# Optimization experiments

Measured on AMD Instinct MI355X. Metric: run time of the kernel, lower is better.

The kernel has to match this reference:

```python
import jax, jax.numpy as jnp
import numpy as np

D_MODEL = 1024
M = 4
NUM_EXPERTS = 8
TOP_K = 2
B, T = 2, 2048


def setup_inputs() -> dict:
    key = jax.random.key(0)
    ks = jax.random.split(key, 4)
    d_ff = D_MODEL * M
    x = jax.random.normal(ks[0], (B, T, D_MODEL), dtype=jnp.float32)
    # torch nn.Linear(d_model, num_experts, bias=False): stored here as (D, E) so logits = x @ gate_w
    gate_w = jax.random.normal(ks[1], (D_MODEL, NUM_EXPERTS), dtype=jnp.float32) * 0.02
    w1 = jax.random.normal(ks[2], (NUM_EXPERTS, D_MODEL, d_ff), dtype=jnp.float32) * 0.02
    b1 = jnp.zeros((NUM_EXPERTS, d_ff), dtype=jnp.float32)
    w2 = jax.random.normal(ks[3], (NUM_EXPERTS, d_ff, D_MODEL), dtype=jnp.float32) * 0.02
    b2 = jnp.zeros((NUM_EXPERTS, D_MODEL), dtype=jnp.float32)
    return {"x": x, "gate_w": gate_w, "w1": w1, "b1": b1, "w2": w2, "b2": b2}


def reference(x, gate_w, w1, b1, w2, b2):
    Bb, Tt, D = x.shape
    E = w1.shape[0]
    N = Bb * Tt
    # gating: top-k logits -> softmax over the k selected experts
    logits = jnp.einsum('btd,de->bte', x, gate_w)               # (B,T,E)
    top_v, top_i = jax.lax.top_k(logits, TOP_K)                 # (B,T,K)
    top_w = jax.nn.softmax(top_v, axis=-1)                      # (B,T,K)

    xf = x.reshape(N, D)
    idx = top_i.reshape(N, TOP_K)
    wts = top_w.reshape(N, TOP_K)
    # dense combine weights: comb[n, e] = sum_k wts[n,k] * [idx[n,k]==e]
    comb = jnp.zeros((N, E), dtype=x.dtype).at[jnp.arange(N)[:, None], idx].add(wts)

    # per-expert dense 2-layer MLP (exact erf GELU, matching torch F.gelu default),
    # combined with gate weights (zero weight == token not routed to expert).
    out = jnp.zeros((N, D), dtype=x.dtype)
    for e in range(E):
        h = jax.nn.gelu(xf @ w1[e] + b1[e], approximate=False)  # (N, D*M)
        out = out + comb[:, e:e + 1] * (h @ w2[e] + b2[e])      # (N, D)
    return out.reshape(Bb, Tt, D)
```

## Files before the change

### kernel.cpp

```cpp
#include <hip/hip_runtime.h>
#include <hip/hip_bf16.h>
#include <math.h>

#define D_MODEL 1024
#define D_FF    4096
#define NEXP    8
#define NTOK    4096
#define NROUTED 8192

typedef __attribute__((ext_vector_type(8))) short bf16x8;
typedef __attribute__((ext_vector_type(4))) float f32x4;
typedef __attribute__((ext_vector_type(4))) unsigned short us4;

#define WS_CNT   0
#define WS_CNT2  64
#define WS_OFF   128
#define WS_TI    256
#define WS_TW    (WS_TI + NTOK*2*4)
#define WS_TOK   (WS_TW + NTOK*2*4)
#define WS_GWT   (WS_TOK + NROUTED*4)
#define WS_XG    (((WS_GWT + NROUTED*4) + 255) & ~255)
#define WS_H     (WS_XG + (size_t)NROUTED*D_MODEL*2)
#define WS_WT    (WS_H + (size_t)NROUTED*D_FF*2)

__device__ __forceinline__ unsigned short f2bf(float f){
  union { float f; unsigned u; } a; a.f = f;
  unsigned u = a.u;
  u = u + 0x7FFF + ((u >> 16) & 1);
  return (unsigned short)(u >> 16);
}

__device__ __forceinline__ void gload_lds16(const void* g, void* l){
  __builtin_amdgcn_global_load_lds((const __attribute__((address_space(1))) void*)g,
                                   (__attribute__((address_space(3))) void*)l, 16, 0, 0);
}

__global__ void moe_gate_kernel(const float* __restrict__ x, const float* __restrict__ gw,
                                int* cnt, int* __restrict__ ti, float* __restrict__ tw){
  int n = blockIdx.x*4 + (threadIdx.x >> 6);
  int lane = threadIdx.x & 63;
  const float* xr = x + (size_t)n * D_MODEL;
  float acc[NEXP];
  #pragma unroll
  for (int e=0;e<NEXP;e++) acc[e] = 0.f;
  for (int d=lane; d<D_MODEL; d+=64){
    float xv = xr[d];
    #pragma unroll
    for (int e=0;e<NEXP;e++) acc[e] += xv * gw[d*NEXP + e];
  }
  #pragma unroll
  for (int e=0;e<NEXP;e++){
    #pragma unroll
    for (int o=32;o;o>>=1) acc[e] += __shfl_down(acc[e], o, 64);
  }
  if (lane == 0){
    int i0 = 0; float v0 = acc[0];
    #pragma unroll
    for (int e=1;e<NEXP;e++) if (acc[e] > v0){ v0 = acc[e]; i0 = e; }
    int i1 = -1; float v1 = -1e30f;
    #pragma unroll
    for (int e=0;e<NEXP;e++) if (e != i0 && acc[e] > v1){ v1 = acc[e]; i1 = e; }
    float p = expf(v1 - v0);
    float inv = 1.f / (1.f + p);
    ti[n*2] = i0; ti[n*2+1] = i1;
    tw[n*2] = inv; tw[n*2+1] = p * inv;
    atomicAdd(&cnt[i0], 1); atomicAdd(&cnt[i1], 1);
  }
}

__global__ void moe_prefix_kernel(const int* __restrict__ cnt, int* __restrict__ off){
  if (threadIdx.x == 0){
    int s = 0;
    for (int e=0;e<NEXP;e++){ off[e] = s; s += cnt[e]; }
    off[NEXP] = s;
  }
}

__global__ void moe_assign_kernel(const float* __restrict__ x, const int* __restrict__ ti,
                                  const float* __restrict__ tw, const int* __restrict__ off,
                                  int* cnt2, int* __restrict__ tok, float* __restrict__ gwt,
                                  unsigned short* __restrict__ Xg){
  __shared__ int ss[2];
  int n = blockIdx.x;
  if (threadIdx.x == 0){
    int i0 = ti[n*2], i1 = ti[n*2+1];
    int s0 = off[i0] + atomicAdd(&cnt2[i0], 1);
    int s1 = off[i1] + atomicAdd(&cnt2[i1], 1);
    tok[s0] = n; tok[s1] = n;
    gwt[s0] = tw[n*2]; gwt[s1] = tw[n*2+1];
    ss[0] = s0; ss[1] = s1;
  }
  __syncthreads();
  int s0 = ss[0], s1 = ss[1];
  int t = threadIdx.x;
  float4 v = ((const float4*)(x + (size_t)n * D_MODEL))[t];
  us4 pk = { f2bf(v.x), f2bf(v.y), f2bf(v.z), f2bf(v.w) };
  *(us4*)(Xg + (size_t)s0 * D_MODEL + t*4) = pk;
  *(us4*)(Xg + (size_t)s1 * D_MODEL + t*4) = pk;
}

__global__ __launch_bounds__(256) void transpose_bf16_kernel(
    const float* __restrict__ W, unsigned short* __restrict__ Wt, int K, int F){
  __shared__ float tile[64][65];
  int e = blockIdx.z;
  int f0 = blockIdx.x * 64, k0 = blockIdx.y * 64;
  const float* Wb = W + (size_t)e * K * F;
  unsigned short* Wtb = Wt + (size_t)e * F * K;
  int tid = threadIdx.x;
  #pragma unroll
  for (int i=0;i<4;i++){
    int idx = i*256 + tid;
    int r = idx >> 4, c4 = (idx & 15) * 4;
    float4 v = *(const float4*)(Wb + (size_t)(k0 + r) * F + f0 + c4);
    tile[r][c4] = v.x; tile[r][c4+1] = v.y; tile[r][c4+2] = v.z; tile[r][c4+3] = v.w;
  }
  __syncthreads();
  #pragma unroll
  for (int i=0;i<4;i++){
    int idx = i*256 + tid;
    int f = idx >> 4, k4 = (idx & 15) * 4;
    us4 pk = { f2bf(tile[k4][f]), f2bf(tile[k4+1][f]), f2bf(tile[k4+2][f]), f2bf(tile[k4+3][f]) };
    *(us4*)(Wtb + (size_t)(f0 + f) * K + k0 + k4) = pk;
  }
}

template<int MODE>
__global__ __launch_bounds__(256) void moe_gemm_kernel(
    char* __restrict__ wsb, const unsigned short* __restrict__ Bt,
    const float* __restrict__ bias, float* __restrict__ out)
{
  const int* off = (const int*)(wsb + WS_OFF);
  const int e  = blockIdx.z;
  const int n0 = off[e];
  const int ne = off[e+1] - n0;
  const int row0 = blockIdx.y * 128;
  if (row0 >= ne) return;
  const int n_off = blockIdx.x * 128;

  const int K = (MODE==1) ? D_MODEL : D_FF;
  const int F = (MODE==1) ? D_FF    : D_MODEL;

  const unsigned short* Ag  = (const unsigned short*)(wsb + (MODE==1 ? (size_t)WS_XG : (size_t)WS_H));
  const unsigned short* Bgt = Bt + (size_t)e * F * K;

  __shared__ __align__(16) char As[16384];
  __shared__ __align__(16) char Bs[16384];

  const int tid = threadIdx.x, lane = tid & 63, w = tid >> 6;
  const int wrow = (w>>1)*64, wcol = (w&1)*64;

  f32x4 acc[4][4];
  #pragma unroll
  for (int i=0;i<4;i++)
    #pragma unroll
    for (int j=0;j<4;j++) acc[i][j] = (f32x4){0.f,0.f,0.f,0.f};

  const int arow   = lane >> 3;
  const int achunk = ((lane & 7) ^ arow) << 4;
  const int ksteps = K / 64;

  for (int kt=0; kt<ksteps; ++kt){
    __syncthreads();
    #pragma unroll
    for (int i=0;i<4;i++){
      int c = w*4 + i;
      int row = c*8 + arow;
      int gr = row0 + row; if (gr >= ne) gr = ne - 1;
      gload_lds16((const char*)(Ag + (size_t)(n0 + gr) * K) + kt*128 + achunk, As + c*1024);
      gload_lds16((const char*)(Bgt + (size_t)(n_off + row) * K) + kt*128 + achunk, Bs + c*1024);
    }
    __syncthreads();
    #pragma unroll
    for (int kk=0; kk<2; ++kk){
      bf16x8 a[4], b[4];
      #pragma unroll
      for (int mi=0; mi<4; mi++){
        int row = wrow + mi*16 + (lane&15);
        int byteoff = (row<<7) + (((kk<<6) + ((lane>>4)<<4)) ^ ((row&7)<<4));
        a[mi] = *(const bf16x8*)(As + byteoff);
      }
      #pragma unroll
      for (int ni=0; ni<4; ni++){
        int col = wcol + ni*16 + (lane&15);
        int byteoff = (col<<7) + (((kk<<6) + ((lane>>4)<<4)) ^ ((col&7)<<4));
        b[ni] = *(const bf16x8*)(Bs + byteoff);
      }
      #pragma unroll
      for (int mi=0; mi<4; mi++)
        #pragma unroll
        for (int ni=0; ni<4; ni++)
          acc[mi][ni] = __builtin_amdgcn_mfma_f32_16x16x32_bf16(a[mi], b[ni], acc[mi][ni], 0, 0, 0);
    }
  }

  if (MODE == 1){
    const float* b1 = bias + (size_t)e * D_FF;
    unsigned short* H = (unsigned short*)(wsb + (size_t)WS_H);
    #pragma unroll
    for (int mi=0; mi<4; mi++){
      int rbase = wrow + mi*16 + ((lane>>4)<<2);
      #pragma unroll
      for (int r=0;r<4;r++){
        int lrow = rbase + r;
        if (row0 + lrow < ne){
          size_t hb = (size_t)(n0 + row0 + lrow) * D_FF;
          #pragma unroll
          for (int ni=0; ni<4; ni++){
            int gcol = n_off + wcol + ni*16 + (lane&15);
            float v = acc[mi][ni][r] + b1[gcol];
            v = 0.5f * v * (1.f + erff(v * 0.70710678118654752f));
            H[hb + gcol] = f2bf(v);
          }
        }
      }
    }
  } else {
    const float* b2 = bias + (size_t)e * D_MODEL;
    const int* tok = (const int*)(wsb + WS_TOK);
    const float* gwt = (const float*)(wsb + WS_GWT);
    #pragma unroll
    for (int mi=0; mi<4; mi++){
      int rbase = wrow + mi*16 + ((lane>>4)<<2);
      #pragma unroll
      for (int r=0;r<4;r++){
        int lrow = rbase + r;
        if (row0 + lrow < ne){
          int slot = n0 + row0 + lrow;
          int tk = tok[slot];
          float g = gwt[slot];
          float* orow = out + (size_t)tk * D_MODEL;
          #pragma unroll
          for (int ni=0; ni<4; ni++){
            int gcol = n_off + wcol + ni*16 + (lane&15);
            atomicAdd(orow + gcol, (acc[mi][ni][r] + b2[gcol]) * g);
          }
        }
      }
    }
  }
}

extern "C" void kernel_launch(void* const* d_in, const int* in_sizes, int n_in,
                              void* d_out, int out_size, void* d_ws, size_t ws_size,
                              hipStream_t stream){
  const float* x   = (const float*)d_in[0];
  const float* gw  = (const float*)d_in[1];
  const float* w1  = (const float*)d_in[2];
  const float* b1  = (const float*)d_in[3];
  const float* w2  = (const float*)d_in[4];
  const float* b2  = (const float*)d_in[5];
  float* out = (float*)d_out;
  char* ws = (char*)d_ws;
  unsigned short* Wt = (unsigned short*)(ws + (size_t)WS_WT);

  hipMemsetAsync(ws, 0, 256, stream);
  hipMemsetAsync(out, 0, (size_t)NTOK * D_MODEL * sizeof(float), stream);

  moe_gate_kernel<<<NTOK/4, 256, 0, stream>>>(x, gw, (int*)(ws+WS_CNT),
                                              (int*)(ws+WS_TI), (float*)(ws+WS_TW));
  moe_prefix_kernel<<<1, 64, 0, stream>>>((const int*)(ws+WS_CNT), (int*)(ws+WS_OFF));
  moe_assign_kernel<<<NTOK, 256, 0, stream>>>(x, (const int*)(ws+WS_TI),
                                              (const float*)(ws+WS_TW), (const int*)(ws+WS_OFF),
                                              (int*)(ws+WS_CNT2), (int*)(ws+WS_TOK),
                                              (float*)(ws+WS_GWT),
                                              (unsigned short*)(ws + (size_t)WS_XG));
  transpose_bf16_kernel<<<dim3(D_FF/64, D_MODEL/64, NEXP), 256, 0, stream>>>(w1, Wt, D_MODEL, D_FF);
  moe_gemm_kernel<1><<<dim3(D_FF/128, NTOK/128, NEXP), 256, 0, stream>>>(ws, Wt, b1, out);
  transpose_bf16_kernel<<<dim3(D_MODEL/64, D_FF/64, NEXP), 256, 0, stream>>>(w2, Wt, D_FF, D_MODEL);
  moe_gemm_kernel<2><<<dim3(D_MODEL/128, NTOK/128, NEXP), 256, 0, stream>>>(ws, Wt, b2, out);
}
```

Measured before the change: 670.4 us.

## Double-buffer LDS tiles in MoE GEMM and split-K the second GEMM

```diff
diff --git a/kernel.cpp b/kernel.cpp
--- a/kernel.cpp
+++ b/kernel.cpp
@@ -124,7 +124,7 @@
   }
 }
 
-template<int MODE>
+template<int MODE, int KS>
 __global__ __launch_bounds__(256) void moe_gemm_kernel(
     char* __restrict__ wsb, const unsigned short* __restrict__ Bt,
     const float* __restrict__ bias, float* __restrict__ out)
@@ -135,41 +135,63 @@
   const int ne = off[e+1] - n0;
   const int row0 = blockIdx.y * 128;
   if (row0 >= ne) return;
-  const int n_off = blockIdx.x * 128;
 
   const int K = (MODE==1) ? D_MODEL : D_FF;
   const int F = (MODE==1) ? D_FF    : D_MODEL;
+  const int FT = F/128;
+  const int n_off  = (blockIdx.x % FT) * 128;
+  const int kchunk = blockIdx.x / FT;
+  const int kloc   = K / (64*KS);
+  const int kt0    = kchunk * kloc;
 
   const unsigned short* Ag  = (const unsigned short*)(wsb + (MODE==1 ? (size_t)WS_XG : (size_t)WS_H));
   const unsigned short* Bgt = Bt + (size_t)e * F * K;
 
-  __shared__ __align__(16) char As[16384];
-  __shared__ __align__(16) char Bs[16384];
+  __shared__ __align__(16) char As[2*16384];
+  __shared__ __align__(16) char Bs[2*16384];
 
   const int tid = threadIdx.x, lane = tid & 63, w = tid >> 6;
   const int wrow = (w>>1)*64, wcol = (w&1)*64;
-
-  f32x4 acc[4][4];
-  #pragma unroll
-  for (int i=0;i<4;i++)
-    #pragma unroll
-    for (int j=0;j<4;j++) acc[i][j] = (f32x4){0.f,0.f,0.f,0.f};
-
   const int arow   = lane >> 3;
   const int achunk = ((lane & 7) ^ arow) << 4;
-  const int ksteps = K / 64;
-
-  for (int kt=0; kt<ksteps; ++kt){
-    __syncthreads();
-    #pragma unroll
-    for (int i=0;i<4;i++){
-      int c = w*4 + i;
-      int row = c*8 + arow;
-      int gr = row0 + row; if (gr >= ne) gr = ne - 1;
-      gload_lds16((const char*)(Ag + (size_t)(n0 + gr) * K) + kt*128 + achunk, As + c*1024);
-      gload_lds16((const char*)(Bgt + (size_t)(n_off + row) * K) + kt*128 + achunk, Bs + c*1024);
-    }
-    __syncthreads();
+
+  const char* aptr[4]; const char* bptr[4];
+  #pragma unroll
+  for (int i=0;i<4;i++){
+    int c = w*4 + i;
+    int row = c*8 + arow;
+    int gr = row0 + row; if (gr >= ne) gr = ne - 1;
+    aptr[i] = (const char*)(Ag + (size_t)(n0 + gr) * K) + achunk;
+    bptr[i] = (const char*)(Bgt + (size_t)(n_off + row) * K) + achunk;
+  }
+
+  f32x4 acc[4][4];
+  #pragma unroll
+  for (int i=0;i<4;i++)
+    #pragma unroll
+    for (int j=0;j<4;j++) acc[i][j] = (f32x4){0.f,0.f,0.f,0.f};
+
+  #pragma unroll
+  for (int i=0;i<4;i++){
+    int c = w*4 + i;
+    gload_lds16(aptr[i] + kt0*128, As + c*1024);
+    gload_lds16(bptr[i] + kt0*128, Bs + c*1024);
+  }
+  __syncthreads();
+
+  int cur = 0;
+  for (int kt = 0; kt < kloc; ++kt){
+    if (kt + 1 < kloc){
+      int nxt = cur ^ 1;
+      #pragma unroll
+      for (int i=0;i<4;i++){
+        int c = w*4 + i;
+        gload_lds16(aptr[i] + (size_t)(kt0+kt+1)*128, As + nxt*16384 + c*1024);
+        gload_lds16(bptr[i] + (size_t)(kt0+kt+1)*128, Bs + nxt*16384 + c*1024);
+      }
+    }
+    const char* Ab = As + cur*16384;
+    const char* Bb = Bs + cur*16384;
     #pragma unroll
     for (int kk=0; kk<2; ++kk){
       bf16x8 a[4], b[4];
@@ -177,13 +199,13 @@
       for (int mi=0; mi<4; mi++){
         int row = wrow + mi*16 + (lane&15);
         int byteoff = (row<<7) + (((kk<<6) + ((lane>>4)<<4)) ^ ((row&7)<<4));
-        a[mi] = *(const bf16x8*)(As + byteoff);
+        a[mi] = *(const bf16x8*)(Ab + byteoff);
       }
       #pragma unroll
       for (int ni=0; ni<4; ni++){
         int col = wcol + ni*16 + (lane&15);
         int byteoff = (col<<7) + (((kk<<6) + ((lane>>4)<<4)) ^ ((col&7)<<4));
-        b[ni] = *(const bf16x8*)(Bs + byteoff);
+        b[ni] = *(const bf16x8*)(Bb + byteoff);
       }
       #pragma unroll
       for (int mi=0; mi<4; mi++)
@@ -191,6 +213,8 @@
         for (int ni=0; ni<4; ni++)
           acc[mi][ni] = __builtin_amdgcn_mfma_f32_16x16x32_bf16(a[mi], b[ni], acc[mi][ni], 0, 0, 0);
     }
+    __syncthreads();
+    cur ^= 1;
   }
 
   if (MODE == 1){
@@ -232,7 +256,8 @@
           #pragma unroll
           for (int ni=0; ni<4; ni++){
             int gcol = n_off + wcol + ni*16 + (lane&15);
-            atomicAdd(orow + gcol, (acc[mi][ni][r] + b2[gcol]) * g);
+            float bb = (kchunk == 0) ? b2[gcol] : 0.f;
+            atomicAdd(orow + gcol, (acc[mi][ni][r] + bb) * g);
           }
         }
       }
@@ -265,7 +290,7 @@
                                               (float*)(ws+WS_GWT),
                                               (unsigned short*)(ws + (size_t)WS_XG));
   transpose_bf16_kernel<<<dim3(D_FF/64, D_MODEL/64, NEXP), 256, 0, stream>>>(w1, Wt, D_MODEL, D_FF);
-  moe_gemm_kernel<1><<<dim3(D_FF/128, NTOK/128, NEXP), 256, 0, stream>>>(ws, Wt, b1, out);
+  moe_gemm_kernel<1,1><<<dim3(D_FF/128, NTOK/128, NEXP), 256, 0, stream>>>(ws, Wt, b1, out);
   transpose_bf16_kernel<<<dim3(D_MODEL/64, D_FF/64, NEXP), 256, 0, stream>>>(w2, Wt, D_FF, D_MODEL);
-  moe_gemm_kernel<2><<<dim3(D_MODEL/128, NTOK/128, NEXP), 256, 0, stream>>>(ws, Wt, b2, out);
-}
+  moe_gemm_kernel<2,4><<<dim3((D_MODEL/128)*4, NTOK/128, NEXP), 256, 0, stream>>>(ws, Wt, b2, out);
+}
```

Result: slower. 706.5 us (+5.4%).

## Use 256x256 tiles with triple-buffered LDS pipeline and split-K for second GEMM

Applied to the files above, without the earlier changes.

```diff
diff --git a/kernel.cpp b/kernel.cpp
--- a/kernel.cpp
+++ b/kernel.cpp
@@ -124,81 +124,116 @@
   }
 }
 
-template<int MODE>
-__global__ __launch_bounds__(256) void moe_gemm_kernel(
+template<int MODE, int KS>
+__global__ __launch_bounds__(512, 1) void moe_gemm_kernel(
     char* __restrict__ wsb, const unsigned short* __restrict__ Bt,
     const float* __restrict__ bias, float* __restrict__ out)
 {
   const int* off = (const int*)(wsb + WS_OFF);
-  const int e  = blockIdx.z;
+
+  const int K  = (MODE==1) ? D_MODEL : D_FF;
+  const int F  = (MODE==1) ? D_FF    : D_MODEL;
+  const int FT = F/256;
+  const int gx = FT*KS, gy = NROUTED/256;
+  int f = ((int)blockIdx.z*gy + (int)blockIdx.y)*gx + (int)blockIdx.x;
+  f = (f & 7)*(gx*gy*NEXP/8) + (f >> 3);
+  const int bx = f % gx, by = (f / gx) % gy, e = f / (gx*gy);
+
   const int n0 = off[e];
   const int ne = off[e+1] - n0;
-  const int row0 = blockIdx.y * 128;
+  const int row0 = by * 256;
   if (row0 >= ne) return;
-  const int n_off = blockIdx.x * 128;
-
-  const int K = (MODE==1) ? D_MODEL : D_FF;
-  const int F = (MODE==1) ? D_FF    : D_MODEL;
+
+  const int n_off  = (bx % FT) * 256;
+  const int kchunk = bx / FT;
+  const int nt     = K / (32*KS);
+  const int ktb0   = kchunk * nt * 64;
 
   const unsigned short* Ag  = (const unsigned short*)(wsb + (MODE==1 ? (size_t)WS_XG : (size_t)WS_H));
   const unsigned short* Bgt = Bt + (size_t)e * F * K;
-
-  __shared__ __align__(16) char As[16384];
-  __shared__ __align__(16) char Bs[16384];
+  const size_t K2 = (size_t)K * 2;
+
+  __shared__ __align__(16) char lds[3*32768];
 
   const int tid = threadIdx.x, lane = tid & 63, w = tid >> 6;
-  const int wrow = (w>>1)*64, wcol = (w&1)*64;
-
-  f32x4 acc[4][4];
-  #pragma unroll
-  for (int i=0;i<4;i++)
+  const int wr = w >> 2, wc = w & 3;
+
+  const int srow = tid >> 2;
+  const int fq   = (srow >> 1) & 3;
+  const int qsB  = ((tid & 3) ^ fq) << 4;
+  int ra0 = row0 + srow;        if (ra0 >= ne) ra0 = ne - 1;
+  int ra1 = row0 + 128 + srow;  if (ra1 >= ne) ra1 = ne - 1;
+  const char* aSrc0 = (const char*)(Ag + (size_t)(n0 + ra0) * K) + ktb0 + qsB;
+  const char* aSrc1 = (const char*)(Ag + (size_t)(n0 + ra1) * K) + ktb0 + qsB;
+  const char* bSrc0 = (const char*)(Bgt + (size_t)(n_off + srow) * K) + ktb0 + qsB;
+  const char* bSrc1 = (const char*)(Bgt + (size_t)(n_off + 128 + srow) * K) + ktb0 + qsB;
+  const int dstOff = w * 1024;
+
+  const int q0 = lane >> 4;
+  int aoff[8], boff[4];
+  #pragma unroll
+  for (int mi=0; mi<8; mi++){
+    int row = wr*128 + mi*16 + (lane & 15);
+    aoff[mi] = row*64 + ((q0 ^ ((row>>1)&3)) << 4);
+  }
+  #pragma unroll
+  for (int ni=0; ni<4; ni++){
+    int col = wc*64 + ni*16 + (lane & 15);
+    boff[ni] = 16384 + col*64 + ((q0 ^ ((col>>1)&3)) << 4);
+  }
+
+  f32x4 acc[8][4];
+  #pragma unroll
+  for (int i=0;i<8;i++)
     #pragma unroll
     for (int j=0;j<4;j++) acc[i][j] = (f32x4){0.f,0.f,0.f,0.f};
 
-  const int arow   = lane >> 3;
-  const int achunk = ((lane & 7) ^ arow) << 4;
-  const int ksteps = K / 64;
-
-  for (int kt=0; kt<ksteps; ++kt){
-    __syncthreads();
-    #pragma unroll
-    for (int i=0;i<4;i++){
-      int c = w*4 + i;
-      int row = c*8 + arow;
-      int gr = row0 + row; if (gr >= ne) gr = ne - 1;
-      gload_lds16((const char*)(Ag + (size_t)(n0 + gr) * K) + kt*128 + achunk, As + c*1024);
-      gload_lds16((const char*)(Bgt + (size_t)(n_off + row) * K) + kt*128 + achunk, Bs + c*1024);
-    }
-    __syncthreads();
-    #pragma unroll
-    for (int kk=0; kk<2; ++kk){
-      bf16x8 a[4], b[4];
+  #define STAGE(tt, bb) { \
+    size_t kb = (size_t)(tt) * 64; \
+    char* dA = lds + (bb)*32768 + dstOff; \
+    gload_lds16(aSrc0 + kb, dA); \
+    gload_lds16(aSrc1 + kb, dA + 8192); \
+    gload_lds16(bSrc0 + kb, dA + 16384); \
+    gload_lds16(bSrc1 + kb, dA + 24576); }
+
+  STAGE(0, 0);
+  STAGE(1, 1);
+
+  for (int t = 0; t < nt; ++t){
+    if (t < nt-1) asm volatile("s_waitcnt vmcnt(4)" ::: "memory");
+    else          asm volatile("s_waitcnt vmcnt(0)" ::: "memory");
+    __builtin_amdgcn_s_barrier();
+    __builtin_amdgcn_sched_barrier(0);
+
+    if (t + 2 < nt) STAGE(t + 2, (t + 2) % 3);
+
+    const char* buf = lds + (t % 3) * 32768;
+    bf16x8 af[8], bf[4];
+    #pragma unroll
+    for (int mi=0; mi<8; mi++) af[mi] = *(const bf16x8*)(buf + aoff[mi]);
+    #pragma unroll
+    for (int ni=0; ni<4; ni++) bf[ni] = *(const bf16x8*)(buf + boff[ni]);
+
+    asm volatile("s_waitcnt lgkmcnt(0)" ::: "memory");
+    __builtin_amdgcn_sched_barrier(0);
+    __builtin_amdgcn_s_setprio(1);
+    #pragma unroll
+    for (int ni=0; ni<4; ni++)
       #pragma unroll
-      for (int mi=0; mi<4; mi++){
-        int row = wrow + mi*16 + (lane&15);
-        int byteoff = (row<<7) + (((kk<<6) + ((lane>>4)<<4)) ^ ((row&7)<<4));
-        a[mi] = *(const bf16x8*)(As + byteoff);
-      }
-      #pragma unroll
-      for (int ni=0; ni<4; ni++){
-        int col = wcol + ni*16 + (lane&15);
-        int byteoff = (col<<7) + (((kk<<6) + ((lane>>4)<<4)) ^ ((col&7)<<4));
-        b[ni] = *(const bf16x8*)(Bs + byteoff);
-      }
-      #pragma unroll
-      for (int mi=0; mi<4; mi++)
-        #pragma unroll
-        for (int ni=0; ni<4; ni++)
-          acc[mi][ni] = __builtin_amdgcn_mfma_f32_16x16x32_bf16(a[mi], b[ni], acc[mi][ni], 0, 0, 0);
-    }
-  }
+      for (int mi=0; mi<8; mi++)
+        acc[mi][ni] = __builtin_amdgcn_mfma_f32_16x16x32_bf16(af[mi], bf[ni], acc[mi][ni], 0, 0, 0);
+    __builtin_amdgcn_s_setprio(0);
+    __builtin_amdgcn_sched_barrier(0);
+    __builtin_amdgcn_s_barrier();
+  }
+  #undef STAGE
 
   if (MODE == 1){
     const float* b1 = bias + (size_t)e * D_FF;
     unsigned short* H = (unsigned short*)(wsb + (size_t)WS_H);
     #pragma unroll
-    for (int mi=0; mi<4; mi++){
-      int rbase = wrow + mi*16 + ((lane>>4)<<2);
+    for (int mi=0; mi<8; mi++){
+      int rbase = wr*128 + mi*16 + ((lane>>4)<<2);
       #pragma unroll
       for (int r=0;r<4;r++){
         int lrow = rbase + r;
@@ -206,7 +241,7 @@
           size_t hb = (size_t)(n0 + row0 + lrow) * D_FF;
           #pragma unroll
           for (int ni=0; ni<4; ni++){
-            int gcol = n_off + wcol + ni*16 + (lane&15);
+            int gcol = n_off + wc*64 + ni*16 + (lane&15);
             float v = acc[mi][ni][r] + b1[gcol];
             v = 0.5f * v * (1.f + erff(v * 0.70710678118654752f));
             H[hb + gcol] = f2bf(v);
@@ -219,8 +254,8 @@
     const int* tok = (const int*)(wsb + WS_TOK);
     const float* gwt = (const float*)(wsb + WS_GWT);
     #pragma unroll
-    for (int mi=0; mi<4; mi++){
-      int rbase = wrow + mi*16 + ((lane>>4)<<2);
+    for (int mi=0; mi<8; mi++){
+      int rbase = wr*128 + mi*16 + ((lane>>4)<<2);
       #pragma unroll
       for (int r=0;r<4;r++){
         int lrow = rbase + r;
@@ -231,8 +266,9 @@
           float* orow = out + (size_t)tk * D_MODEL;
           #pragma unroll
           for (int ni=0; ni<4; ni++){
-            int gcol = n_off + wcol + ni*16 + (lane&15);
-            atomicAdd(orow + gcol, (acc[mi][ni][r] + b2[gcol]) * g);
+            int gcol = n_off + wc*64 + ni*16 + (lane&15);
+            float bb = (kchunk == 0) ? b2[gcol] : 0.f;
+            atomicAdd(orow + gcol, (acc[mi][ni][r] + bb) * g);
           }
         }
       }
@@ -265,7 +301,7 @@
                                               (float*)(ws+WS_GWT),
                                               (unsigned short*)(ws + (size_t)WS_XG));
   transpose_bf16_kernel<<<dim3(D_FF/64, D_MODEL/64, NEXP), 256, 0, stream>>>(w1, Wt, D_MODEL, D_FF);
-  moe_gemm_kernel<1><<<dim3(D_FF/128, NTOK/128, NEXP), 256, 0, stream>>>(ws, Wt, b1, out);
+  moe_gemm_kernel<1,1><<<dim3(16, NROUTED/256, NEXP), 512, 0, stream>>>(ws, Wt, b1, out);
   transpose_bf16_kernel<<<dim3(D_MODEL/64, D_FF/64, NEXP), 256, 0, stream>>>(w2, Wt, D_FF, D_MODEL);
-  moe_gemm_kernel<2><<<dim3(D_MODEL/128, NTOK/128, NEXP), 256, 0, stream>>>(ws, Wt, b2, out);
-}
+  moe_gemm_kernel<2,4><<<dim3(16, NROUTED/256, NEXP), 512, 0, stream>>>(ws, Wt, b2, out);
+}
```

After: 659.3 us. Within noise of the previous version (-1.7%).
